# Optimization experiments

Hardware: AMD Instinct MI355X
Metric: run time of the kernel (lower is better)

The kernel has to match this reference:

```python
import jax, jax.numpy as jnp
import numpy as np

N, E = 10000, 160000
B, F, P, C = 16, 2, 12, 32


def gcn_norm(edge_index, edge_weight, n):
    # GCN symmetric normalization with self-loops (fill value 1.0, improved=False)
    src, dst = edge_index[0], edge_index[1]
    loop = jnp.arange(n, dtype=src.dtype)
    src = jnp.concatenate([src, loop])
    dst = jnp.concatenate([dst, loop])
    w = jnp.concatenate([edge_weight, jnp.ones((n,), edge_weight.dtype)])
    deg = jnp.zeros((n,), w.dtype).at[dst].add(w)
    dinv = jnp.where(deg > 0, jax.lax.rsqrt(deg), 0.0)
    return src, dst, dinv[src] * w * dinv[dst]


def gcn_conv(x, W, b, src, dst, norm, n):
    # x: [B, N, Fin] -> [B, N, Fout]; transform-then-propagate like GCNConv
    xw = x @ W
    msgs = xw[:, src, :] * norm[None, :, None]  # gather over source nodes
    out = jnp.zeros((x.shape[0], n, W.shape[1]), x.dtype).at[:, dst].add(msgs)
    return out + b


def setup_inputs():
    key = jax.random.key(0)
    ks = jax.random.split(key, 20)
    s = 0.1
    return {
        "x": jax.random.normal(ks[0], (B, N, F, P), jnp.float32),
        "edge_index": jax.random.randint(ks[1], (2, E), 0, N, jnp.int32),
        "edge_weight": jax.random.uniform(ks[2], (E,), jnp.float32),
        "W_z": jax.random.normal(ks[3], (F, C), jnp.float32) * s,
        "b_z": jnp.zeros((C,), jnp.float32),
        "lin_z_W": jax.random.normal(ks[4], (2 * C, C), jnp.float32) * s,
        "lin_z_b": jnp.zeros((C,), jnp.float32),
        "W_r": jax.random.normal(ks[5], (F, C), jnp.float32) * s,
        "b_r": jnp.zeros((C,), jnp.float32),
        "lin_r_W": jax.random.normal(ks[6], (2 * C, C), jnp.float32) * s,
        "lin_r_b": jnp.zeros((C,), jnp.float32),
        "W_h": jax.random.normal(ks[7], (F, C), jnp.float32) * s,
        "b_h": jnp.zeros((C,), jnp.float32),
        "lin_h_W": jax.random.normal(ks[8], (2 * C, C), jnp.float32) * s,
        "lin_h_b": jnp.zeros((C,), jnp.float32),
        "attention": jax.random.uniform(ks[9], (P,), jnp.float32),
        "lin_out_W": jax.random.normal(ks[10], (C, P), jnp.float32) * s,
        "lin_out_b": jnp.zeros((P,), jnp.float32),
    }


def reference(x, edge_index, edge_weight, W_z, b_z, lin_z_W, lin_z_b, W_r, b_r,
              lin_r_W, lin_r_b, W_h, b_h, lin_h_W, lin_h_b, attention,
              lin_out_W, lin_out_b):
    b, n, f, p = x.shape
    c = W_z.shape[1]
    src, dst, norm = gcn_norm(edge_index, edge_weight, n)
    probs = jax.nn.softmax(attention)  # attention over periods
    H0 = jnp.zeros((b, n, c), x.dtype)  # A3TGCN2 passes H=None each period
    xs = jnp.moveaxis(x, 3, 0)  # [P, B, N, F]

    def step(acc, inp):
        xp, w = inp  # xp: [B, N, F]
        Gz = gcn_conv(xp, W_z, b_z, src, dst, norm, n)
        Z = jax.nn.sigmoid(jnp.concatenate([Gz, H0], -1) @ lin_z_W + lin_z_b)
        Gr = gcn_conv(xp, W_r, b_r, src, dst, norm, n)
        R = jax.nn.sigmoid(jnp.concatenate([Gr, H0], -1) @ lin_r_W + lin_r_b)
        Gh = gcn_conv(xp, W_h, b_h, src, dst, norm, n)
        Ht = jnp.tanh(jnp.concatenate([Gh, H0 * R], -1) @ lin_h_W + lin_h_b)
        Hn = Z * H0 + (1.0 - Z) * Ht  # one GRU step from zero hidden
        return acc + w * Hn, None

    H_acc, _ = jax.lax.scan(step, H0, (xs, probs))
    h = jax.nn.relu(H_acc)
    return h @ lin_out_W + lin_out_b  # [B, N, periods]
```

## Files before the change

### kernel.cpp

```cpp
#include <hip/hip_runtime.h>
#include <hip/hip_bf16.h>

#define NN 10000
#define EE 160000
#define BB 16
#define PP 12
#define CC 32
#define CAP 64
#define NCB 313
#define NHB 625

__device__ __forceinline__ float fast_rcp(float x){ return __builtin_amdgcn_rcpf(x); }
__device__ __forceinline__ float fast_exp2(float x){
#if __has_builtin(__builtin_amdgcn_exp2f)
    return __builtin_amdgcn_exp2f(x);
#else
    return exp2f(x);
#endif
}
__device__ __forceinline__ unsigned short f2bfu(float f){
    union { float f; unsigned int i; } c; c.f = f;
    unsigned int r = c.i + 0x7FFFu + ((c.i >> 16) & 1u);
    return (unsigned short)(r >> 16);
}
__device__ __forceinline__ void up2(unsigned int u, float& a, float& b){
    union { unsigned int i; float f; } c;
    c.i = u << 16;          a = c.f;
    c.i = u & 0xFFFF0000u;  b = c.f;
}
__device__ __forceinline__ void unp24(uint4 q0, uint4 q1, uint4 q2, float* f){
    up2(q0.x,f[0],f[1]);   up2(q0.y,f[2],f[3]);   up2(q0.z,f[4],f[5]);   up2(q0.w,f[6],f[7]);
    up2(q1.x,f[8],f[9]);   up2(q1.y,f[10],f[11]); up2(q1.z,f[12],f[13]); up2(q1.w,f[14],f[15]);
    up2(q2.x,f[16],f[17]); up2(q2.y,f[18],f[19]); up2(q2.z,f[20],f[21]); up2(q2.w,f[22],f[23]);
}

__global__ __launch_bounds__(256) void k_stage(const float* __restrict__ x,
        const int* __restrict__ srcI, const int* __restrict__ dstI,
        const float* __restrict__ ew,
        unsigned short* __restrict__ xc, float* __restrict__ deg, int* __restrict__ cnt,
        int2* __restrict__ bucket, const int* __restrict__ canary_p,
        const float* __restrict__ Wz, const float* __restrict__ bz,
        const float* __restrict__ LzW, const float* __restrict__ lzb,
        const float* __restrict__ Wh, const float* __restrict__ bh,
        const float* __restrict__ LhW, const float* __restrict__ lhb,
        const float* __restrict__ att, const float* __restrict__ LoW,
        const float* __restrict__ lob, float* __restrict__ wbuf){
    __shared__ unsigned short tile[32*400];
    int bid = blockIdx.x, tid = threadIdx.x;
    if (bid < NCB){
        int n0 = bid*32;
        int n1 = NN - n0; if (n1 > 32) n1 = 32;
        int tot = 16 * n1 * 6;
        for (int i = tid; i < tot; i += 256){
            int b = i / (n1*6);
            int r = i - b*(n1*6);
            float4 f = *(const float4*)(x + b*(NN*24) + n0*24 + r*4);
            ushort4 v; v.x=f2bfu(f.x); v.y=f2bfu(f.y); v.z=f2bfu(f.z); v.w=f2bfu(f.w);
            int nl = (r*4) / 24;
            int fp = (r*4) - nl*24;
            ((ushort4*)tile)[nl*100 + (b*24 + fp)/4] = v;
        }
        __syncthreads();
        int tot4 = n1*48;
        const uint4* t4 = (const uint4*)tile;
        uint4* dst4 = (uint4*)(xc + n0*384);
        for (int i = tid; i < tot4; i += 256){
            int nl = i/48, j = i - nl*48;
            dst4[i] = t4[nl*50 + j];
        }
    } else if (bid < NCB + NHB){
        int canary = *canary_p;
        int e = (bid - NCB)*256 + tid;
        int d = dstI[e];
        float w = ew[e];
        atomicAdd(&deg[d], w);
        int rk = atomicAdd(&cnt[d], 1) - canary;
        bucket[d*CAP + rk] = make_int2(srcI[e], __float_as_int(w));
    } else {
        const float L2E = 1.4426950408889634f;
        int c = tid;
        if (c < CC){
            float s0=0.f,s1=0.f,sb=lzb[c], h0=0.f,h1=0.f,hb=lhb[c];
            for (int k=0;k<CC;k++){
                float wz = LzW[k*CC+c];
                s0 += Wz[k]*wz; s1 += Wz[CC+k]*wz; sb += bz[k]*wz;
                float wh = LhW[k*CC+c];
                h0 += Wh[k]*wh; h1 += Wh[CC+k]*wh; hb += bh[k]*wh;
            }
            float* wp = wbuf + c*8;
            wp[0]=s0*L2E; wp[1]=s1*L2E; wp[2]=sb*L2E;
            wp[3]=h0*(2.f*L2E); wp[4]=h1*(2.f*L2E); wp[5]=hb*(2.f*L2E);
            wp[6]=0.f; wp[7]=0.f;
            for (int q=0;q<PP;q++) wbuf[288 + c*PP + q] = LoW[c*PP+q];
        } else if (c == 32){
            float a[PP]; float m = -1e30f;
            for (int p=0;p<PP;p++){ a[p]=att[p]; m = fmaxf(m, a[p]); }
            float s=0.f;
            for (int p=0;p<PP;p++){ a[p]=__expf(a[p]-m); s += a[p]; }
            float r = 1.f/s;
            for (int p=0;p<PP;p++) wbuf[256+p] = a[p]*r;
        } else if (c == 33){
            for (int q=0;q<PP;q++) wbuf[268+q] = lob[q];
        }
    }
}

__global__ __launch_bounds__(128, 4) void k_fused(const unsigned short* __restrict__ xc,
        const int2* __restrict__ bucket, const int* __restrict__ cnt,
        const float* __restrict__ deg, const float* __restrict__ wbuf,
        const int* __restrict__ canary_p, float* __restrict__ out){
    int tid  = threadIdx.x;
    int half = tid >> 6;
    int lane = tid & 63;
    int h    = lane >> 3;
    int b    = (lane & 7) | (half << 3);
    int n    = blockIdx.x;
    const unsigned short* xl = xc + b*24;

    int len = cnt[n] - *canary_p;
    float dd = rsqrtf(deg[n] + 1.0f);

    int2 be = bucket[n*CAP + lane];
    int   ecol = (lane < len) ? be.x : n;
    float ewv  = (lane < len) ? __int_as_float(be.y)
               : (lane == len ? 1.0f : 0.0f);
    float ev   = rsqrtf(deg[ecol] + 1.0f) * ewv * dd;

    float acc[24];
    #pragma unroll
    for (int k=0;k<24;k++) acc[k] = 0.f;

    int lim = len + 1;
    for (int eb = 0; eb < lim; eb += 16){
        int e1 = eb + h, e2 = eb + h + 8;
        int   c1 = __shfl(ecol, e1, 64);
        float v1 = __shfl(ev,   e1, 64);
        int   c2 = __shfl(ecol, e2, 64);
        float v2 = __shfl(ev,   e2, 64);
        const uint4* p1 = (const uint4*)(xl + c1*384);
        const uint4* p2 = (const uint4*)(xl + c2*384);
        uint4 qa0=p1[0], qa1=p1[1], qa2=p1[2];
        uint4 qb0=p2[0], qb1=p2[1], qb2=p2[2];
        float fa[24], fb[24];
        unp24(qa0,qa1,qa2,fa);
        unp24(qb0,qb1,qb2,fb);
        #pragma unroll
        for (int k=0;k<24;k++) acc[k] = fmaf(v1, fa[k], fmaf(v2, fb[k], acc[k]));
    }
    #pragma unroll
    for (int k=0;k<24;k++) acc[k] += __shfl_xor(acc[k], 8, 64);
    #pragma unroll
    for (int k=0;k<24;k++) acc[k] += __shfl_xor(acc[k], 16, 64);
    #pragma unroll
    for (int k=0;k<24;k++) acc[k] += __shfl_xor(acc[k], 32, 64);

    float pr[12];
    #pragma unroll
    for (int p=0;p<12;p++) pr[p] = wbuf[256+p];
    float o[12];
    #pragma unroll
    for (int q=0;q<12;q++) o[q] = 0.f;
    const float4* wp = (const float4*)wbuf;
    int cbase = h*4;
    #pragma unroll
    for (int cc=0; cc<4; ++cc){
        int c = cbase + cc;
        float4 wa = wp[c*2];
        float4 wb = wp[c*2+1];
        float a = 0.f;
        #pragma unroll
        for (int p=0;p<12;p++){
            float y0 = acc[p], y1 = acc[12+p];
            float zs = fmaf(y1, wa.y, fmaf(y0, wa.x, wa.z));
            float hs = fmaf(y1, wb.x, fmaf(y0, wa.w, wb.y));
            hs = fminf(hs, 80.f);
            float ez = fast_exp2(zs);
            float eh = fast_exp2(hs);
            float den = fmaf(ez, eh, ez) + (eh + 1.f);
            float t  = fast_rcp(den);
            a = fmaf(pr[p]*(eh-1.f), t, a);
        }
        a = fmaxf(a, 0.f);
        const float4* lw = (const float4*)(wbuf + 288 + c*12);
        float4 w0 = lw[0], w1 = lw[1], w2 = lw[2];
        o[0]=fmaf(a,w0.x,o[0]); o[1]=fmaf(a,w0.y,o[1]); o[2] =fmaf(a,w0.z,o[2]);  o[3] =fmaf(a,w0.w,o[3]);
        o[4]=fmaf(a,w1.x,o[4]); o[5]=fmaf(a,w1.y,o[5]); o[6] =fmaf(a,w1.z,o[6]);  o[7] =fmaf(a,w1.w,o[7]);
        o[8]=fmaf(a,w2.x,o[8]); o[9]=fmaf(a,w2.y,o[9]); o[10]=fmaf(a,w2.z,o[10]); o[11]=fmaf(a,w2.w,o[11]);
    }
    #pragma unroll
    for (int q=0;q<12;q++) o[q] += __shfl_xor(o[q], 8, 64);
    #pragma unroll
    for (int q=0;q<12;q++) o[q] += __shfl_xor(o[q], 16, 64);
    #pragma unroll
    for (int q=0;q<12;q++) o[q] += __shfl_xor(o[q], 32, 64);
    #pragma unroll
    for (int q=0;q<12;q++) o[q] += wbuf[268+q];
    if (h < 3){
        float4* op = (float4*)(out + (b*NN + n)*12);
        op[h] = make_float4(o[h*4], o[h*4+1], o[h*4+2], o[h*4+3]);
    }
}

extern "C" void kernel_launch(void* const* d_in, const int* in_sizes, int n_in,
                              void* d_out, int out_size, void* d_ws, size_t ws_size,
                              hipStream_t stream) {
    const float* x   = (const float*)d_in[0];
    const int*   ei  = (const int*)d_in[1];
    const float* ew  = (const float*)d_in[2];
    const float* Wz  = (const float*)d_in[3];
    const float* bz  = (const float*)d_in[4];
    const float* LzW = (const float*)d_in[5];
    const float* lzb = (const float*)d_in[6];
    const float* Wh  = (const float*)d_in[11];
    const float* bh  = (const float*)d_in[12];
    const float* LhW = (const float*)d_in[13];
    const float* lhb = (const float*)d_in[14];
    const float* att = (const float*)d_in[15];
    const float* LoW = (const float*)d_in[16];
    const float* lob = (const float*)d_in[17];
    float* out = (float*)d_out;

    const int* srcI = ei;
    const int* dstI = ei + EE;

    char* ws = (char*)d_ws;
    size_t off = 0;
    auto alloc = [&](size_t bytes){ void* p = ws + off; off += (bytes + 255)/256*256; return p; };
    int*            canary = (int*)alloc(256);
    float*          deg    = (float*)alloc((size_t)NN*4);
    int*            cnt    = (int*)alloc((size_t)NN*4);
    float*          wbuf   = (float*)alloc(672*4);
    unsigned short* xc     = (unsigned short*)alloc((size_t)BB*NN*24*2);
    int2*           bucket = (int2*)alloc((size_t)NN*CAP*8);

    hipLaunchKernelGGL(k_stage, dim3(NCB + NHB + 1), dim3(256), 0, stream,
                       x, srcI, dstI, ew, xc, deg, cnt, bucket, canary,
                       Wz, bz, LzW, lzb, Wh, bh, LhW, lhb, att, LoW, lob, wbuf);
    hipLaunchKernelGGL(k_fused, dim3(NN), dim3(128), 0, stream,
                       xc, bucket, cnt, deg, wbuf, canary, out);
}
```

Baseline: 161.5 us.

## Store staged node features in fp32 instead of bf16 and tighten gather tail

The staging kernel now writes the transposed node-feature buffer as fp32 rather than rounding to bf16, and the fused gather kernel reads fp32 directly, with no bf16 unpacking. The edge loop handles full 16-edge chunks and then a tail of up to two 8-edge half-chunks, so fewer padded rows are read past the real edge count. This improves accuracy and removes the pack/unpack ALU work, but doubles the staging buffer and the bytes moved by the random per-edge gathers.

New measurement: 173.3 us. 7.3% more time.

```diff
diff --git a/kernel.cpp b/kernel.cpp
--- a/kernel.cpp
+++ b/kernel.cpp
@@ -18,26 +18,11 @@
     return exp2f(x);
 #endif
 }
-__device__ __forceinline__ unsigned short f2bfu(float f){
-    union { float f; unsigned int i; } c; c.f = f;
-    unsigned int r = c.i + 0x7FFFu + ((c.i >> 16) & 1u);
-    return (unsigned short)(r >> 16);
-}
-__device__ __forceinline__ void up2(unsigned int u, float& a, float& b){
-    union { unsigned int i; float f; } c;
-    c.i = u << 16;          a = c.f;
-    c.i = u & 0xFFFF0000u;  b = c.f;
-}
-__device__ __forceinline__ void unp24(uint4 q0, uint4 q1, uint4 q2, float* f){
-    up2(q0.x,f[0],f[1]);   up2(q0.y,f[2],f[3]);   up2(q0.z,f[4],f[5]);   up2(q0.w,f[6],f[7]);
-    up2(q1.x,f[8],f[9]);   up2(q1.y,f[10],f[11]); up2(q1.z,f[12],f[13]); up2(q1.w,f[14],f[15]);
-    up2(q2.x,f[16],f[17]); up2(q2.y,f[18],f[19]); up2(q2.z,f[20],f[21]); up2(q2.w,f[22],f[23]);
-}
 
 __global__ __launch_bounds__(256) void k_stage(const float* __restrict__ x,
         const int* __restrict__ srcI, const int* __restrict__ dstI,
         const float* __restrict__ ew,
-        unsigned short* __restrict__ xc, float* __restrict__ deg, int* __restrict__ cnt,
+        float* __restrict__ xc, float* __restrict__ deg, int* __restrict__ cnt,
         int2* __restrict__ bucket, const int* __restrict__ canary_p,
         const float* __restrict__ Wz, const float* __restrict__ bz,
         const float* __restrict__ LzW, const float* __restrict__ lzb,
@@ -45,28 +30,27 @@
         const float* __restrict__ LhW, const float* __restrict__ lhb,
         const float* __restrict__ att, const float* __restrict__ LoW,
         const float* __restrict__ lob, float* __restrict__ wbuf){
-    __shared__ unsigned short tile[32*400];
+    __shared__ float tile[32*388];
     int bid = blockIdx.x, tid = threadIdx.x;
     if (bid < NCB){
         int n0 = bid*32;
         int n1 = NN - n0; if (n1 > 32) n1 = 32;
         int tot = 16 * n1 * 6;
+        float4* t4 = (float4*)tile;
         for (int i = tid; i < tot; i += 256){
             int b = i / (n1*6);
             int r = i - b*(n1*6);
             float4 f = *(const float4*)(x + b*(NN*24) + n0*24 + r*4);
-            ushort4 v; v.x=f2bfu(f.x); v.y=f2bfu(f.y); v.z=f2bfu(f.z); v.w=f2bfu(f.w);
             int nl = (r*4) / 24;
             int fp = (r*4) - nl*24;
-            ((ushort4*)tile)[nl*100 + (b*24 + fp)/4] = v;
+            t4[nl*97 + (b*24 + fp)/4] = f;
         }
         __syncthreads();
-        int tot4 = n1*48;
-        const uint4* t4 = (const uint4*)tile;
-        uint4* dst4 = (uint4*)(xc + n0*384);
+        int tot4 = n1*96;
+        float4* dst4 = (float4*)(xc + (size_t)n0*384);
         for (int i = tid; i < tot4; i += 256){
-            int nl = i/48, j = i - nl*48;
-            dst4[i] = t4[nl*50 + j];
+            int nl = i/96, j = i - nl*96;
+            dst4[i] = t4[nl*97 + j];
         }
     } else if (bid < NCB + NHB){
         int canary = *canary_p;
@@ -105,7 +89,19 @@
     }
 }
 
-__global__ __launch_bounds__(128, 4) void k_fused(const unsigned short* __restrict__ xc,
+__device__ __forceinline__ void gather24(const float* __restrict__ xl, int col,
+                                         float v, float* __restrict__ acc){
+    const float4* p = (const float4*)(xl + (size_t)col*384);
+    float4 q0=p[0], q1=p[1], q2=p[2], q3=p[3], q4=p[4], q5=p[5];
+    acc[0] =fmaf(v,q0.x,acc[0]);  acc[1] =fmaf(v,q0.y,acc[1]);  acc[2] =fmaf(v,q0.z,acc[2]);  acc[3] =fmaf(v,q0.w,acc[3]);
+    acc[4] =fmaf(v,q1.x,acc[4]);  acc[5] =fmaf(v,q1.y,acc[5]);  acc[6] =fmaf(v,q1.z,acc[6]);  acc[7] =fmaf(v,q1.w,acc[7]);
+    acc[8] =fmaf(v,q2.x,acc[8]);  acc[9] =fmaf(v,q2.y,acc[9]);  acc[10]=fmaf(v,q2.z,acc[10]); acc[11]=fmaf(v,q2.w,acc[11]);
+    acc[12]=fmaf(v,q3.x,acc[12]); acc[13]=fmaf(v,q3.y,acc[13]); acc[14]=fmaf(v,q3.z,acc[14]); acc[15]=fmaf(v,q3.w,acc[15]);
+    acc[16]=fmaf(v,q4.x,acc[16]); acc[17]=fmaf(v,q4.y,acc[17]); acc[18]=fmaf(v,q4.z,acc[18]); acc[19]=fmaf(v,q4.w,acc[19]);
+    acc[20]=fmaf(v,q5.x,acc[20]); acc[21]=fmaf(v,q5.y,acc[21]); acc[22]=fmaf(v,q5.z,acc[22]); acc[23]=fmaf(v,q5.w,acc[23]);
+}
+
+__global__ __launch_bounds__(128, 4) void k_fused(const float* __restrict__ xc,
         const int2* __restrict__ bucket, const int* __restrict__ cnt,
         const float* __restrict__ deg, const float* __restrict__ wbuf,
         const int* __restrict__ canary_p, float* __restrict__ out){
@@ -115,7 +111,7 @@
     int h    = lane >> 3;
     int b    = (lane & 7) | (half << 3);
     int n    = blockIdx.x;
-    const unsigned short* xl = xc + b*24;
+    const float* xl = xc + b*24;
 
     int len = cnt[n] - *canary_p;
     float dd = rsqrtf(deg[n] + 1.0f);
@@ -131,21 +127,26 @@
     for (int k=0;k<24;k++) acc[k] = 0.f;
 
     int lim = len + 1;
-    for (int eb = 0; eb < lim; eb += 16){
+    int eb = 0;
+    for (; eb + 16 <= lim; eb += 16){
         int e1 = eb + h, e2 = eb + h + 8;
         int   c1 = __shfl(ecol, e1, 64);
         float v1 = __shfl(ev,   e1, 64);
         int   c2 = __shfl(ecol, e2, 64);
         float v2 = __shfl(ev,   e2, 64);
-        const uint4* p1 = (const uint4*)(xl + c1*384);
-        const uint4* p2 = (const uint4*)(xl + c2*384);
-        uint4 qa0=p1[0], qa1=p1[1], qa2=p1[2];
-        uint4 qb0=p2[0], qb1=p2[1], qb2=p2[2];
-        float fa[24], fb[24];
-        unp24(qa0,qa1,qa2,fa);
-        unp24(qb0,qb1,qb2,fb);
-        #pragma unroll
-        for (int k=0;k<24;k++) acc[k] = fmaf(v1, fa[k], fmaf(v2, fb[k], acc[k]));
+        gather24(xl, c1, v1, acc);
+        gather24(xl, c2, v2, acc);
+    }
+    if (eb < lim){
+        int   c1 = __shfl(ecol, eb + h, 64);
+        float v1 = __shfl(ev,   eb + h, 64);
+        gather24(xl, c1, v1, acc);
+        eb += 8;
+    }
+    if (eb < lim){
+        int   c1 = __shfl(ecol, eb + h, 64);
+        float v1 = __shfl(ev,   eb + h, 64);
+        gather24(xl, c1, v1, acc);
     }
     #pragma unroll
     for (int k=0;k<24;k++) acc[k] += __shfl_xor(acc[k], 8, 64);
@@ -226,12 +227,12 @@
     char* ws = (char*)d_ws;
     size_t off = 0;
     auto alloc = [&](size_t bytes){ void* p = ws + off; off += (bytes + 255)/256*256; return p; };
-    int*            canary = (int*)alloc(256);
-    float*          deg    = (float*)alloc((size_t)NN*4);
-    int*            cnt    = (int*)alloc((size_t)NN*4);
-    float*          wbuf   = (float*)alloc(672*4);
-    unsigned short* xc     = (unsigned short*)alloc((size_t)BB*NN*24*2);
-    int2*           bucket = (int2*)alloc((size_t)NN*CAP*8);
+    int*    canary = (int*)alloc(256);
+    float*  deg    = (float*)alloc((size_t)NN*4);
+    int*    cnt    = (int*)alloc((size_t)NN*4);
+    float*  wbuf   = (float*)alloc(672*4);
+    float*  xc     = (float*)alloc((size_t)BB*NN*24*4);
+    int2*   bucket = (int2*)alloc((size_t)NN*CAP*8);
 
     hipLaunchKernelGGL(k_stage, dim3(NCB + NHB + 1), dim3(256), 0, stream,
                        x, srcI, dstI, ew, xc, deg, cnt, bucket, canary,
```
